# Kernel tuning notes

Measured on AMD Instinct MI355X. Metric: run time of the kernel, lower is better.

The kernel has to match this reference:

```python
import math
import jax, jax.numpy as jnp
import numpy as np

B, N, D = 16, 4096, 256
N_CAT, N_TPC, N_VPT, N_SP = 16, 8, 4, 16
N_TYPE = N_CAT * N_TPC          # 128
N_VAR = N_TYPE * N_VPT          # 512
THRESH = 0.1
MASK_VAL = jnp.finfo(jnp.float32).min / 2


def _linear(x, w, b):
    # torch nn.Linear: y = x @ W^T + b, W: (out, in)
    return x @ w.T + b


def _level(codes, proj_w, proj_b, K, X, mask, tau):
    """One codebook level: attention of codes over tokens.
    codes: (M, d). Returns H:(B,M,d), w_raw:(B,M)."""
    Q = _linear(codes, proj_w, proj_b)                       # (M, d)
    attn = jnp.einsum('md,bnd->bmn', Q, K) / math.sqrt(D)    # (B, M, N)
    attn = jnp.where(mask[:, None, :], attn, MASK_VAL)
    attn = jnp.clip(attn, -50.0, 50.0)
    G = jnp.nan_to_num(jax.nn.softmax(attn, axis=-1))        # (B, M, N)
    H = jnp.einsum('bmn,bnd->bmd', G, X)                     # (B, M, d)
    w_raw = jnp.linalg.norm(H, axis=-1) / tau                # (B, M)
    return H, w_raw


def _sparsify(w, thr):
    ws = jnp.where(w > thr, w, 0.0)
    return ws / (ws.sum(axis=-1, keepdims=True) + 1e-8)


def _forward(X, positions, category_codes, type_codes, variant_codes,
             spatial_codes, log_tau, cat_w, cat_b, type_w, type_b,
             var_w, var_b, sp_w, sp_b, k_w, k_b, g1_w, g1_b, g2_w, g2_b,
             out_w, out_b, ln_g, ln_b, level_weights, mask):
    tau = jnp.clip(jnp.exp(log_tau[0]) + 0.1, 0.1, 2.0)
    K = _linear(X, k_w, k_b)                                 # (B, N, d)

    # Level 0: category
    H_cat, w_cat_raw = _level(category_codes, cat_w, cat_b, K, X, mask, tau)
    w_cat = jax.nn.softmax(w_cat_raw, axis=-1)
    w_cat_sp = _sparsify(w_cat, THRESH)

    # Level 1: type, gated by category selection
    H_type, w_type_raw = _level(type_codes.reshape(-1, D), type_w, type_b,
                                K, X, mask, tau)
    w_t = (w_type_raw.reshape(-1, N_CAT, N_TPC) * w_cat_sp[:, :, None]
           ).reshape(-1, N_TYPE)
    w_type = jax.nn.softmax(w_t, axis=-1)
    w_type_sp = _sparsify(w_type, THRESH / 2)

    # Level 2: variant, gated by type selection
    H_var, w_var_raw = _level(variant_codes.reshape(-1, D), var_w, var_b,
                              K, X, mask, tau)
    w_type_exp = jnp.repeat(w_type_sp, N_VPT, axis=-1)       # (B, 512)
    w_var = jax.nn.softmax(w_var_raw * w_type_exp, axis=-1)
    w_var_sp = _sparsify(w_var, THRESH / 4)

    # Spatial level (independent)
    H_sp, w_sp_raw = _level(spatial_codes, sp_w, sp_b, K, X, mask, tau)
    w_sp = jax.nn.softmax(w_sp_raw, axis=-1)
    w_sp_sp = _sparsify(w_sp, THRESH)

    z_cat = jnp.einsum('bm,bmd->bd', w_cat_sp, H_cat)
    z_type = jnp.einsum('bm,bmd->bd', w_type_sp, H_type)
    z_var = jnp.einsum('bm,bmd->bd', w_var_sp, H_var)
    z_spatial = jnp.einsum('bm,bmd->bd', w_sp_sp, H_sp)

    # Position gating of category summary
    mask_f = mask.astype(X.dtype)[:, :, None]
    pos_pooled = (positions * mask_f).sum(1) / jnp.maximum(mask_f.sum(1), 1.0)
    gate_in = jnp.concatenate([z_cat, pos_pooled], axis=-1)  # (B, 2d)
    h = jax.nn.gelu(_linear(gate_in, g1_w, g1_b), approximate=False)
    pos_gate = jax.nn.sigmoid(_linear(h, g2_w, g2_b))
    z_cat = z_cat * pos_gate

    # Learned level combine + gated output projection
    lw = jax.nn.softmax(level_weights)
    z = (lw[0] * z_cat + lw[1] * z_type + lw[2] * z_var + lw[3] * z_spatial)
    z = _linear(z, out_w, out_b)
    mu = z.mean(-1, keepdims=True)
    var = z.var(-1, keepdims=True)
    z = (z - mu) / jnp.sqrt(var + 1e-5) * ln_g + ln_b
    return z


def setup_inputs() -> dict:
    key = jax.random.key(0)
    ks = jax.random.split(key, 32)
    s = 1.0 / math.sqrt(D)
    inp = {
        'X': jax.random.normal(ks[0], (B, N, D), jnp.float32),
        'positions': jax.random.normal(ks[1], (B, N, D), jnp.float32),
        'category_codes': jax.random.normal(ks[2], (N_CAT, D)) * 0.02,
        'type_codes': jax.random.normal(ks[3], (N_CAT, N_TPC, D)) * 0.02,
        'variant_codes': jax.random.normal(ks[4], (N_CAT, N_TPC, N_VPT, D)) * 0.02,
        'spatial_codes': jax.random.normal(ks[5], (N_SP, D)) * 0.02,
        'log_tau': jnp.zeros((1,), jnp.float32),
        'cat_w': jax.random.normal(ks[6], (D, D)) * s,
        'cat_b': jnp.zeros((D,)),
        'type_w': jax.random.normal(ks[7], (D, D)) * s,
        'type_b': jnp.zeros((D,)),
        'var_w': jax.random.normal(ks[8], (D, D)) * s,
        'var_b': jnp.zeros((D,)),
        'sp_w': jax.random.normal(ks[9], (D, D)) * s,
        'sp_b': jnp.zeros((D,)),
        'k_w': jax.random.normal(ks[10], (D, D)) * s,
        'k_b': jnp.zeros((D,)),
        'g1_w': jax.random.normal(ks[11], (D, 2 * D)) * s,
        'g1_b': jnp.zeros((D,)),
        'g2_w': jax.random.normal(ks[12], (D, D)) * s,
        'g2_b': jnp.zeros((D,)),
        'out_w': jax.random.normal(ks[13], (D, D)) * s,
        'out_b': jnp.zeros((D,)),
        'ln_g': jnp.ones((D,)),
        'ln_b': jnp.zeros((D,)),
        'level_weights': jnp.ones((4,)) / 4.0,
        'mask': jnp.ones((B, N), jnp.bool_),
    }
    return inp


def reference(X, positions, category_codes, type_codes, variant_codes,
              spatial_codes, log_tau, cat_w, cat_b, type_w, type_b,
              var_w, var_b, sp_w, sp_b, k_w, k_b, g1_w, g1_b, g2_w, g2_b,
              out_w, out_b, ln_g, ln_b, level_weights, mask):
    return _forward(X, positions, category_codes, type_codes, variant_codes,
                    spatial_codes, log_tau, cat_w, cat_b, type_w, type_b,
                    var_w, var_b, sp_w, sp_b, k_w, k_b, g1_w, g1_b,
                    g2_w, g2_b, out_w, out_b, ln_g, ln_b, level_weights, mask)
```

## Files before the change

### kernel.cpp

```cpp
#include <hip/hip_runtime.h>


#define DEV static __device__ __forceinline__

typedef short bf16x8 __attribute__((ext_vector_type(8)));
typedef float f32x4 __attribute__((ext_vector_type(4)));
typedef unsigned short u16x8 __attribute__((ext_vector_type(8)));

DEV float bf2f(unsigned short u) {
  return __uint_as_float(((unsigned int)u) << 16);
}
DEV unsigned short f2bf(float f) {
  unsigned int x = __float_as_uint(f);
  unsigned int r = (x + 0x7fffu + ((x >> 16) & 1u)) >> 16;
  return (unsigned short)r;
}

DEV void gl2lds16(const void* g, void* l) {
  __builtin_amdgcn_global_load_lds(
      (const __attribute__((address_space(1))) unsigned int*)g,
      (__attribute__((address_space(3))) unsigned int*)l, 16, 0, 0);
}

DEV bf16x8 pack8(const float4 a, const float4 b) {
  bf16x8 r;
  r[0] = (short)f2bf(a.x); r[1] = (short)f2bf(a.y);
  r[2] = (short)f2bf(a.z); r[3] = (short)f2bf(a.w);
  r[4] = (short)f2bf(b.x); r[5] = (short)f2bf(b.y);
  r[6] = (short)f2bf(b.z); r[7] = (short)f2bf(b.w);
  return r;
}

DEV size_t pk_off(int rt, int ks) { return ((size_t)rt * 8 + ks) * 512; }

__global__ __launch_bounds__(256) void kproj_mfma(
    const float* __restrict__ X, const float* __restrict__ W,
    const float* __restrict__ bias, unsigned short* __restrict__ Kp) {
  __shared__ __align__(16) unsigned short As[128 * 72];
  __shared__ __align__(16) unsigned short Bs[128 * 72];
  const int m0 = blockIdx.x * 128, c0 = blockIdx.y * 128;
  const int t = threadIdx.x, l = t & 63, w = t >> 6;
  const int wm = (w & 1) * 64, wn = (w >> 1) * 64;
  const f32x4 zero = {0.f, 0.f, 0.f, 0.f};
  f32x4 acc[4][4];
#pragma unroll
  for (int i = 0; i < 4; ++i)
#pragma unroll
    for (int j = 0; j < 4; ++j) acc[i][j] = zero;
  const int rr = t >> 3, cc = (t & 7) * 8;
  for (int kc = 0; kc < 256; kc += 64) {
    __syncthreads();
#pragma unroll
    for (int p = 0; p < 4; ++p) {
      const int r = p * 32 + rr;
      const float* xs = &X[(size_t)(m0 + r) * 256 + kc + cc];
      const float4 a0 = *(const float4*)&xs[0];
      const float4 a1 = *(const float4*)&xs[4];
      *(bf16x8*)&As[r * 72 + cc] = pack8(a0, a1);
      const float* wsrc = &W[(size_t)(c0 + r) * 256 + kc + cc];
      const float4 b0 = *(const float4*)&wsrc[0];
      const float4 b1 = *(const float4*)&wsrc[4];
      *(bf16x8*)&Bs[r * 72 + cc] = pack8(b0, b1);
    }
    __syncthreads();
#pragma unroll
    for (int ks = 0; ks < 2; ++ks) {
      const int koff = ks * 32 + ((l >> 4) & 3) * 8;
      bf16x8 a[4], b[4];
#pragma unroll
      for (int f = 0; f < 4; ++f)
        a[f] = *(const bf16x8*)&As[(wm + f * 16 + (l & 15)) * 72 + koff];
#pragma unroll
      for (int f = 0; f < 4; ++f)
        b[f] = *(const bf16x8*)&Bs[(wn + f * 16 + (l & 15)) * 72 + koff];
#pragma unroll
      for (int i = 0; i < 4; ++i)
#pragma unroll
        for (int j = 0; j < 4; ++j)
          acc[i][j] =
              __builtin_amdgcn_mfma_f32_16x16x32_bf16(a[i], b[j], acc[i][j],
                                                      0, 0, 0);
    }
  }
  const int q = (l >> 4) & 3;
#pragma unroll
  for (int j = 0; j < 4; ++j) {
    const int c = c0 + wn + j * 16 + (l & 15);
    const float bv = bias[c];
#pragma unroll
    for (int i = 0; i < 4; ++i) {
      const int mrow = m0 + wm + i * 16 + q * 4;
#pragma unroll
      for (int r = 0; r < 4; ++r) {
        const int m = mrow + r;
        Kp[pk_off(m >> 4, c >> 5) + ((m & 15) + 16 * ((c >> 3) & 3)) * 8 +
           (c & 7)] = f2bf(acc[i][j][r] + bv);
      }
    }
  }
}

__global__ __launch_bounds__(256) void xT_kern(const float* __restrict__ X,
                                               unsigned short* __restrict__ XTp) {
  __shared__ float Ls[64][65];
  const int tn = blockIdx.x, td = blockIdx.y, b = blockIdx.z;
  const int t = threadIdx.x;
  const int nl = t >> 2, dp = (t & 3) * 16;
  const float* src =
      X + ((size_t)b * 4096 + tn * 64 + nl) * 256 + td * 64 + dp;
#pragma unroll
  for (int v = 0; v < 4; ++v) {
    const float4 x = *(const float4*)&src[v * 4];
    Ls[nl][dp + v * 4 + 0] = x.x;
    Ls[nl][dp + v * 4 + 1] = x.y;
    Ls[nl][dp + v * 4 + 2] = x.z;
    Ls[nl][dp + v * 4 + 3] = x.w;
  }
  __syncthreads();
  const int dl = t >> 2, np = (t & 3) * 16;
  u16x8 h0, h1;
#pragma unroll
  for (int j = 0; j < 8; ++j) h0[j] = f2bf(Ls[np + j][dl]);
#pragma unroll
  for (int j = 0; j < 8; ++j) h1[j] = f2bf(Ls[np + 8 + j][dl]);
  const int d = td * 64 + dl;
  const int n0g = tn * 64 + np;
  const int n1g = n0g + 8;
  unsigned short* dst = XTp + (size_t)b * 1048576;
  const size_t o0 = (((size_t)(d >> 4) * 128) + (n0g >> 5)) * 512 +
                    ((d & 15) + 16 * ((n0g >> 3) & 3)) * 8;
  const size_t o1 = (((size_t)(d >> 4) * 128) + (n1g >> 5)) * 512 +
                    ((d & 15) + 16 * ((n1g >> 3) & 3)) * 8;
  *(u16x8*)&dst[o0] = h0;
  *(u16x8*)&dst[o1] = h1;
}

__global__ __launch_bounds__(256) void qproj_kern(
    const float* __restrict__ cat_codes, const float* __restrict__ type_codes,
    const float* __restrict__ var_codes, const float* __restrict__ sp_codes,
    const float* __restrict__ cat_w, const float* __restrict__ cat_b,
    const float* __restrict__ type_w, const float* __restrict__ type_b,
    const float* __restrict__ var_w, const float* __restrict__ var_b,
    const float* __restrict__ sp_w, const float* __restrict__ sp_b,
    unsigned short* __restrict__ Qp) {
  const int m = blockIdx.x;
  const int t = threadIdx.x;
  const size_t off = pk_off(m >> 4, t >> 5) +
                     ((m & 15) + 16 * ((t >> 3) & 3)) * 8 + (t & 7);
  if (m >= 672) {
    Qp[off] = 0;
    return;
  }
  const float* code;
  const float* W;
  const float* bias;
  if (m < 16)       { code = cat_codes  + m * 256;         W = cat_w;  bias = cat_b; }
  else if (m < 144) { code = type_codes + (m - 16) * 256;  W = type_w; bias = type_b; }
  else if (m < 656) { code = var_codes  + (m - 144) * 256; W = var_w;  bias = var_b; }
  else              { code = sp_codes   + (m - 656) * 256; W = sp_w;   bias = sp_b; }
  __shared__ float xs[256];
  xs[t] = code[t];
  __syncthreads();
  float a = bias[t];
  const float* wr = W + (size_t)t * 256;
  for (int k = 0; k < 256; k += 4) {
    const float4 w = *(const float4*)&wr[k];
    a = fmaf(w.x, xs[k], a);
    a = fmaf(w.y, xs[k + 1], a);
    a = fmaf(w.z, xs[k + 2], a);
    a = fmaf(w.w, xs[k + 3], a);
  }
  Qp[off] = f2bf(a);
}

__global__ __launch_bounds__(256, 2) void attn_fused(
    const unsigned short* __restrict__ Qp, const unsigned short* __restrict__ Kp,
    const unsigned short* __restrict__ XTp,
    const unsigned char* __restrict__ mask, float* __restrict__ H,
    float* __restrict__ lsum) {
  __shared__ __align__(16) unsigned short Ks[2][16384];
  __shared__ __align__(16) unsigned short Plds[64 * 72];
  __shared__ unsigned char msk[1024];
  const int combo = blockIdx.x;
  const int m0 = blockIdx.y * 64;
  const int b = combo >> 2;
  const int nbase = (combo & 3) * 1024;
  const int t = threadIdx.x, l = t & 63, w = t >> 6;
  const int l15 = l & 15, q = l >> 4;
  ((uchar4*)msk)[t] = ((const uchar4*)(mask + (size_t)b * 4096 + nbase))[t];
  const int mt_g = (m0 >> 4) + w;
  bf16x8 qf[8];
#pragma unroll
  for (int ks = 0; ks < 8; ++ks)
    qf[ks] = *(const bf16x8*)&Qp[pk_off(mt_g, ks) + l * 8];
  const f32x4 zero = {0.f, 0.f, 0.f, 0.f};
  f32x4 accO[4][4];
#pragma unroll
  for (int i = 0; i < 4; ++i)
#pragma unroll
    for (int j = 0; j < 4; ++j) accO[i][j] = zero;
  f32x4 rs = zero;
  const unsigned short* XTb = XTp + (size_t)b * 1048576;
  const unsigned short* Kchunk0 = Kp + ((size_t)b * 256 + (nbase >> 4)) * 4096;
#pragma unroll
  for (int i = 0; i < 8; ++i)
    gl2lds16(Kchunk0 + (w * 8 + i) * 512 + l * 8, &Ks[0][(w * 8 + i) * 512]);
  for (int c = 0; c < 16; ++c) {
    const int cur = c & 1;
    __syncthreads();
    const int nst0 = (nbase >> 5) + c * 2;
    bf16x8 xf[2][4];
#pragma unroll
    for (int ks2 = 0; ks2 < 2; ++ks2)
#pragma unroll
      for (int dj = 0; dj < 4; ++dj)
        xf[ks2][dj] = *(const bf16x8*)&XTb[((size_t)(4 * w + dj) * 128 +
                                            nst0 + ks2) * 512 + l * 8];
    f32x4 accS[4];
#pragma unroll
    for (int f = 0; f < 4; ++f) accS[f] = zero;
#pragma unroll
    for (int ks = 0; ks < 8; ++ks) {
      bf16x8 kf[4];
#pragma unroll
      for (int f = 0; f < 4; ++f)
        kf[f] = *(const bf16x8*)&Ks[cur][(f * 8 + ks) * 512 + l * 8];
#pragma unroll
      for (int f = 0; f < 4; ++f)
        accS[f] = __builtin_amdgcn_mfma_f32_16x16x32_bf16(qf[ks], kf[f],
                                                          accS[f], 0, 0, 0);
    }
#pragma unroll
    for (int f = 0; f < 4; ++f) {
      const bool mk = msk[c * 64 + f * 16 + l15] != 0;
#pragma unroll
      for (int r = 0; r < 4; ++r) {
        float s = accS[f][r] * 0.0625f;
        s = fminf(fmaxf(s, -50.f), 50.f);
        if (!mk) s = -50.f;
        const float e = __expf(s);
        Plds[(w * 16 + q * 4 + r) * 72 + f * 16 + l15] = f2bf(e);
        rs[r] += e;
      }
    }
    __syncthreads();
    if (c < 15) {
      const unsigned short* src = Kchunk0 + (size_t)(c + 1) * 16384;
      unsigned short* dst = &Ks[1 - cur][0];
#pragma unroll
      for (int i = 0; i < 8; ++i)
        gl2lds16(src + (w * 8 + i) * 512 + l * 8, dst + (w * 8 + i) * 512);
    }
#pragma unroll
    for (int ks2 = 0; ks2 < 2; ++ks2) {
      bf16x8 pf[4];
#pragma unroll
      for (int mt = 0; mt < 4; ++mt)
        pf[mt] = *(const bf16x8*)&Plds[(mt * 16 + l15) * 72 + ks2 * 32 + q * 8];
#pragma unroll
      for (int mt = 0; mt < 4; ++mt)
#pragma unroll
        for (int dj = 0; dj < 4; ++dj)
          accO[mt][dj] = __builtin_amdgcn_mfma_f32_16x16x32_bf16(
              pf[mt], xf[ks2][dj], accO[mt][dj], 0, 0, 0);
    }
  }
#pragma unroll
  for (int r = 0; r < 4; ++r) {
    float v = rs[r];
    v += __shfl_xor(v, 1, 64);
    v += __shfl_xor(v, 2, 64);
    v += __shfl_xor(v, 4, 64);
    v += __shfl_xor(v, 8, 64);
    const int m = m0 + w * 16 + q * 4 + r;
    if (l15 == 0 && m < 672) atomicAdd(&lsum[b * 672 + m], v);
  }
#pragma unroll
  for (int mt = 0; mt < 4; ++mt) {
    const int mbase = m0 + mt * 16 + q * 4;
#pragma unroll
    for (int dj = 0; dj < 4; ++dj) {
      const int d = w * 64 + dj * 16 + l15;
#pragma unroll
      for (int r = 0; r < 4; ++r) {
        const int m = mbase + r;
        if (m < 672)
          atomicAdd(&H[((size_t)b * 672 + m) * 256 + d], accO[mt][dj][r]);
      }
    }
  }
}

__global__ __launch_bounds__(256) void hfinal_ip(
    float* __restrict__ H, const float* __restrict__ lsum,
    const float* __restrict__ log_tau, float* __restrict__ wraw) {
  const int bm = blockIdx.x;
  const int t = threadIdx.x;
  __shared__ float red[256];
  const float inv = 1.0f / lsum[bm];
  const float v = H[(size_t)bm * 256 + t] * inv;
  H[(size_t)bm * 256 + t] = v;
  red[t] = v * v;
  __syncthreads();
  for (int s = 128; s > 0; s >>= 1) {
    if (t < s) red[t] += red[t + s];
    __syncthreads();
  }
  if (t == 0) {
    const float tau = fminf(fmaxf(expf(log_tau[0]) + 0.1f, 0.1f), 2.0f);
    wraw[bm] = sqrtf(red[0]) / tau;
  }
}

__global__ __launch_bounds__(256) void pospool_kern(
    const float* __restrict__ pos, const unsigned char* __restrict__ mask,
    float* __restrict__ pacc, float* __restrict__ cnt) {
  const int b = blockIdx.x, seg = blockIdx.y, t = threadIdx.x;
  const int dg = t & 63;
  const int nl = t >> 6;
  const int n0 = seg * 128;
  float4 acc = make_float4(0.f, 0.f, 0.f, 0.f);
  float c = 0.f;
  const float* pb = pos + (size_t)b * 4096 * 256;
  for (int j = 0; j < 32; ++j) {
    const int n = n0 + j * 4 + nl;
    const unsigned char mk = mask[(size_t)b * 4096 + n];
    if (mk) {
      const float4 v = *(const float4*)&pb[(size_t)n * 256 + dg * 4];
      acc.x += v.x; acc.y += v.y; acc.z += v.z; acc.w += v.w;
      if (dg == 0) c += 1.f;
    }
  }
  __shared__ float4 red4[256];
  __shared__ float redc[4];
  red4[t] = acc;
  if (dg == 0) redc[nl] = c;
  __syncthreads();
  if (t < 64) {
    float4 s = red4[t];
    const float4 s1 = red4[t + 64], s2 = red4[t + 128], s3 = red4[t + 192];
    s.x += s1.x + s2.x + s3.x;
    s.y += s1.y + s2.y + s3.y;
    s.z += s1.z + s2.z + s3.z;
    s.w += s1.w + s2.w + s3.w;
    float* pa = pacc + b * 256 + t * 4;
    atomicAdd(pa + 0, s.x);
    atomicAdd(pa + 1, s.y);
    atomicAdd(pa + 2, s.z);
    atomicAdd(pa + 3, s.w);
    if (t == 0) atomicAdd(&cnt[b], redc[0] + redc[1] + redc[2] + redc[3]);
  }
}

DEV float wave_max(float v) {
#pragma unroll
  for (int m = 1; m < 64; m <<= 1) v = fmaxf(v, __shfl_xor(v, m, 64));
  return v;
}
DEV float wave_sum(float v) {
#pragma unroll
  for (int m = 1; m < 64; m <<= 1) v += __shfl_xor(v, m, 64);
  return v;
}

__global__ __launch_bounds__(256) void combine_kern(
    const float* __restrict__ wraw, const float* __restrict__ H,
    float* __restrict__ zbuf) {
  const int b = blockIdx.x, t = threadIdx.x, l = t & 63;
  __shared__ float wr[672];
  __shared__ float wsp[672];
  for (int i = t; i < 672; i += 256) wr[i] = wraw[b * 672 + i];
  __syncthreads();
  {
    const float v = (l < 16) ? wr[l] : -1e30f;
    const float mx = wave_max(v);
    const float e = (l < 16) ? expf(wr[l] - mx) : 0.f;
    const float s = wave_sum(e);
    float w = e / s;
    w = (w > 0.1f) ? w : 0.f;
    const float s2 = wave_sum(w);
    if (l < 16) wsp[l] = w / (s2 + 1e-8f);
  }
  __syncthreads();
  {
    const float L0 = wr[16 + l] * wsp[l >> 3];
    const float L1 = wr[16 + 64 + l] * wsp[(64 + l) >> 3];
    const float mx = wave_max(fmaxf(L0, L1));
    const float e0 = expf(L0 - mx), e1 = expf(L1 - mx);
    const float s = wave_sum(e0 + e1);
    float w0 = e0 / s, w1 = e1 / s;
    w0 = (w0 > 0.05f) ? w0 : 0.f;
    w1 = (w1 > 0.05f) ? w1 : 0.f;
    const float s2 = wave_sum(w0 + w1);
    const float inv2 = 1.f / (s2 + 1e-8f);
    wsp[16 + l] = w0 * inv2;
    wsp[16 + 64 + l] = w1 * inv2;
  }
  __syncthreads();
  {
    float Lv[8];
    float lm = -1e30f;
#pragma unroll
    for (int j = 0; j < 8; ++j) {
      const int i = l * 8 + j;
      Lv[j] = wr[144 + i] * wsp[16 + (i >> 2)];
      lm = fmaxf(lm, Lv[j]);
    }
    const float mx = wave_max(lm);
    float ls = 0.f;
#pragma unroll
    for (int j = 0; j < 8; ++j) {
      Lv[j] = expf(Lv[j] - mx);
      ls += Lv[j];
    }
    const float s = wave_sum(ls);
    const float inv = 1.f / s;
    float ls2 = 0.f;
#pragma unroll
    for (int j = 0; j < 8; ++j) {
      float w = Lv[j] * inv;
      w = (w > 0.025f) ? w : 0.f;
      Lv[j] = w;
      ls2 += w;
    }
    const float s2 = wave_sum(ls2);
    const float inv2 = 1.f / (s2 + 1e-8f);
#pragma unroll
    for (int j = 0; j < 8; ++j) wsp[144 + l * 8 + j] = Lv[j] * inv2;
  }
  __syncthreads();
  {
    const float v = (l < 16) ? wr[656 + l] : -1e30f;
    const float mx = wave_max(v);
    const float e = (l < 16) ? expf(wr[656 + l] - mx) : 0.f;
    const float s = wave_sum(e);
    float w = e / s;
    w = (w > 0.1f) ? w : 0.f;
    const float s2 = wave_sum(w);
    if (l < 16) wsp[656 + l] = w / (s2 + 1e-8f);
  }
  __syncthreads();
  const float* Hb = H + (size_t)b * 672 * 256 + t;
  float z0 = 0.f, z1 = 0.f, z2 = 0.f, z3 = 0.f;
  for (int m = 0; m < 16; ++m) {
    const float wv = wsp[m];
    if (wv != 0.f) z0 = fmaf(wv, Hb[(size_t)m * 256], z0);
  }
  for (int m = 0; m < 128; ++m) {
    const float wv = wsp[16 + m];
    if (wv != 0.f) z1 = fmaf(wv, Hb[(size_t)(16 + m) * 256], z1);
  }
  for (int m = 0; m < 512; ++m) {
    const float wv = wsp[144 + m];
    if (wv != 0.f) z2 = fmaf(wv, Hb[(size_t)(144 + m) * 256], z2);
  }
  for (int m = 0; m < 16; ++m) {
    const float wv = wsp[656 + m];
    if (wv != 0.f) z3 = fmaf(wv, Hb[(size_t)(656 + m) * 256], z3);
  }
  zbuf[(b * 4 + 0) * 256 + t] = z0;
  zbuf[(b * 4 + 1) * 256 + t] = z1;
  zbuf[(b * 4 + 2) * 256 + t] = z2;
  zbuf[(b * 4 + 3) * 256 + t] = z3;
}

__global__ __launch_bounds__(256) void gate_kern(
    const float* __restrict__ zbuf, const float* __restrict__ pacc,
    const float* __restrict__ cnt, const float* __restrict__ g1_w,
    const float* __restrict__ g1_b, const float* __restrict__ g2_w,
    const float* __restrict__ g2_b, const float* __restrict__ out_w,
    const float* __restrict__ out_b, const float* __restrict__ ln_g,
    const float* __restrict__ ln_b, const float* __restrict__ lvlw,
    float* __restrict__ out) {
  const int b = blockIdx.x, t = threadIdx.x;
  __shared__ float gin[512];
  __shared__ float hb[256];
  __shared__ float zc[256];
  __shared__ float red[256];
  const float z0 = zbuf[(b * 4 + 0) * 256 + t];
  gin[t] = z0;
  const float c = fmaxf(cnt[b], 1.0f);
  gin[256 + t] = pacc[b * 256 + t] / c;
  __syncthreads();
  float a = g1_b[t];
  const float* w1 = g1_w + (size_t)t * 512;
  for (int k = 0; k < 512; k += 4) {
    const float4 w = *(const float4*)&w1[k];
    a = fmaf(w.x, gin[k], a);
    a = fmaf(w.y, gin[k + 1], a);
    a = fmaf(w.z, gin[k + 2], a);
    a = fmaf(w.w, gin[k + 3], a);
  }
  const float hg = 0.5f * a * (1.0f + erff(a * 0.7071067811865475f));
  hb[t] = hg;
  __syncthreads();
  float a2 = g2_b[t];
  const float* w2 = g2_w + (size_t)t * 256;
  for (int k = 0; k < 256; k += 4) {
    const float4 w = *(const float4*)&w2[k];
    a2 = fmaf(w.x, hb[k], a2);
    a2 = fmaf(w.y, hb[k + 1], a2);
    a2 = fmaf(w.z, hb[k + 2], a2);
    a2 = fmaf(w.w, hb[k + 3], a2);
  }
  const float pg = 1.0f / (1.0f + expf(-a2));
  const float l0 = lvlw[0], l1 = lvlw[1], l2 = lvlw[2], l3 = lvlw[3];
  const float mx = fmaxf(fmaxf(l0, l1), fmaxf(l2, l3));
  const float e0 = expf(l0 - mx), e1 = expf(l1 - mx);
  const float e2 = expf(l2 - mx), e3 = expf(l3 - mx);
  const float einv = 1.0f / (e0 + e1 + e2 + e3);
  const float zmix = (e0 * z0 * pg + e1 * zbuf[(b * 4 + 1) * 256 + t] +
                      e2 * zbuf[(b * 4 + 2) * 256 + t] +
                      e3 * zbuf[(b * 4 + 3) * 256 + t]) * einv;
  zc[t] = zmix;
  __syncthreads();
  float o = out_b[t];
  const float* wo = out_w + (size_t)t * 256;
  for (int k = 0; k < 256; k += 4) {
    const float4 w = *(const float4*)&wo[k];
    o = fmaf(w.x, zc[k], o);
    o = fmaf(w.y, zc[k + 1], o);
    o = fmaf(w.z, zc[k + 2], o);
    o = fmaf(w.w, zc[k + 3], o);
  }
  red[t] = o;
  __syncthreads();
  for (int s = 128; s > 0; s >>= 1) {
    if (t < s) red[t] += red[t + s];
    __syncthreads();
  }
  const float mu = red[0] / 256.f;
  __syncthreads();
  red[t] = o * o;
  __syncthreads();
  for (int s = 128; s > 0; s >>= 1) {
    if (t < s) red[t] += red[t + s];
    __syncthreads();
  }
  const float var = red[0] / 256.f - mu * mu;
  out[b * 256 + t] = (o - mu) * rsqrtf(var + 1e-5f) * ln_g[t] + ln_b[t];
}

extern "C" void kernel_launch(void* const* d_in, const int* in_sizes, int n_in,
                              void* d_out, int out_size, void* d_ws,
                              size_t ws_size, hipStream_t stream) {
  (void)in_sizes; (void)n_in; (void)out_size; (void)ws_size;
  const float* X          = (const float*)d_in[0];
  const float* positions  = (const float*)d_in[1];
  const float* cat_codes  = (const float*)d_in[2];
  const float* type_codes = (const float*)d_in[3];
  const float* var_codes  = (const float*)d_in[4];
  const float* sp_codes   = (const float*)d_in[5];
  const float* log_tau    = (const float*)d_in[6];
  const float* cat_w      = (const float*)d_in[7];
  const float* cat_b      = (const float*)d_in[8];
  const float* type_w     = (const float*)d_in[9];
  const float* type_b     = (const float*)d_in[10];
  const float* var_w      = (const float*)d_in[11];
  const float* var_b      = (const float*)d_in[12];
  const float* sp_w       = (const float*)d_in[13];
  const float* sp_b       = (const float*)d_in[14];
  const float* k_w        = (const float*)d_in[15];
  const float* k_b        = (const float*)d_in[16];
  const float* g1_w       = (const float*)d_in[17];
  const float* g1_b       = (const float*)d_in[18];
  const float* g2_w       = (const float*)d_in[19];
  const float* g2_b       = (const float*)d_in[20];
  const float* out_w      = (const float*)d_in[21];
  const float* out_b      = (const float*)d_in[22];
  const float* ln_g       = (const float*)d_in[23];
  const float* ln_b       = (const float*)d_in[24];
  const float* lvlw       = (const float*)d_in[25];
  const unsigned char* mask = (const unsigned char*)d_in[26];

  char* ws = (char*)d_ws;
  constexpr size_t O_KP  = 0;
  constexpr size_t O_XT  = 33554432;
  constexpr size_t O_QP  = 67108864;
  constexpr size_t O_H   = 67469312;
  constexpr size_t O_L   = 78479360;
  constexpr size_t O_WR  = 78522368;
  constexpr size_t O_PA  = 78565376;
  constexpr size_t O_CNT = 78581760;
  constexpr size_t O_Z   = 78581824;

  unsigned short* Kp  = (unsigned short*)(ws + O_KP);
  unsigned short* XTp = (unsigned short*)(ws + O_XT);
  unsigned short* Qp  = (unsigned short*)(ws + O_QP);
  float* H            = (float*)(ws + O_H);
  float* lsum         = (float*)(ws + O_L);
  float* wraw         = (float*)(ws + O_WR);
  float* pacc         = (float*)(ws + O_PA);
  float* cnt          = (float*)(ws + O_CNT);
  float* zbuf         = (float*)(ws + O_Z);
  float* out          = (float*)d_out;

  hipMemsetAsync(lsum, 0, 16 * 672 * 4, stream);
  hipMemsetAsync(H, 0, 11010048, stream);
  hipMemsetAsync(pacc, 0, 16 * 256 * 4, stream);
  hipMemsetAsync(cnt, 0, 64, stream);

  qproj_kern<<<dim3(704), 256, 0, stream>>>(
      cat_codes, type_codes, var_codes, sp_codes, cat_w, cat_b, type_w, type_b,
      var_w, var_b, sp_w, sp_b, Qp);
  kproj_mfma<<<dim3(512, 2), 256, 0, stream>>>(X, k_w, k_b, Kp);
  xT_kern<<<dim3(64, 4, 16), 256, 0, stream>>>(X, XTp);
  pospool_kern<<<dim3(16, 32), 256, 0, stream>>>(positions, mask, pacc, cnt);

  attn_fused<<<dim3(64, 11), 256, 0, stream>>>(Qp, Kp, XTp, mask, H, lsum);

  hfinal_ip<<<dim3(16 * 672), 256, 0, stream>>>(H, lsum, log_tau, wraw);
  combine_kern<<<dim3(16), 256, 0, stream>>>(wraw, H, zbuf);
  gate_kern<<<dim3(16), 256, 0, stream>>>(zbuf, pacc, cnt, g1_w, g1_b, g2_w,
                                          g2_b, out_w, out_b, ln_g, ln_b, lvlw,
                                          out);
}
```

Before: 451.2 us.

## Fold softmax normalisation into combine weights and split combine across blocks

Measured after the change: 424.8 us. 5.8% less time.

```diff
diff --git a/kernel.cpp b/kernel.cpp
--- a/kernel.cpp
+++ b/kernel.cpp
@@ -291,24 +291,19 @@
   }
 }
 
-__global__ __launch_bounds__(256) void hfinal_ip(
-    float* __restrict__ H, const float* __restrict__ lsum,
+__global__ __launch_bounds__(256) void hnorm_kern(
+    const float* __restrict__ H, const float* __restrict__ lsum,
     const float* __restrict__ log_tau, float* __restrict__ wraw) {
-  const int bm = blockIdx.x;
-  const int t = threadIdx.x;
-  __shared__ float red[256];
-  const float inv = 1.0f / lsum[bm];
-  const float v = H[(size_t)bm * 256 + t] * inv;
-  H[(size_t)bm * 256 + t] = v;
-  red[t] = v * v;
-  __syncthreads();
-  for (int s = 128; s > 0; s >>= 1) {
-    if (t < s) red[t] += red[t + s];
-    __syncthreads();
-  }
-  if (t == 0) {
+  const int b = blockIdx.x, j = blockIdx.y;
+  const int t = threadIdx.x, l = t & 63, w = t >> 6;
+  const int m = j * 4 + w;
+  const float4 v = *(const float4*)&H[((size_t)b * 672 + m) * 256 + l * 4];
+  float ss = v.x * v.x + v.y * v.y + v.z * v.z + v.w * v.w;
+#pragma unroll
+  for (int s = 1; s < 64; s <<= 1) ss += __shfl_xor(ss, s, 64);
+  if (l == 0) {
     const float tau = fminf(fmaxf(expf(log_tau[0]) + 0.1f, 0.1f), 2.0f);
-    wraw[bm] = sqrtf(red[0]) / tau;
+    wraw[b * 672 + m] = sqrtf(ss) / (lsum[b * 672 + m] * tau);
   }
 }
 
@@ -324,12 +319,13 @@
   const float* pb = pos + (size_t)b * 4096 * 256;
   for (int j = 0; j < 32; ++j) {
     const int n = n0 + j * 4 + nl;
-    const unsigned char mk = mask[(size_t)b * 4096 + n];
-    if (mk) {
-      const float4 v = *(const float4*)&pb[(size_t)n * 256 + dg * 4];
-      acc.x += v.x; acc.y += v.y; acc.z += v.z; acc.w += v.w;
-      if (dg == 0) c += 1.f;
-    }
+    const float mf = mask[(size_t)b * 4096 + n] ? 1.f : 0.f;
+    const float4 v = *(const float4*)&pb[(size_t)n * 256 + dg * 4];
+    acc.x = fmaf(mf, v.x, acc.x);
+    acc.y = fmaf(mf, v.y, acc.y);
+    acc.z = fmaf(mf, v.z, acc.z);
+    acc.w = fmaf(mf, v.w, acc.w);
+    c += mf;
   }
   __shared__ float4 red4[256];
   __shared__ float redc[4];
@@ -364,9 +360,9 @@
 }
 
 __global__ __launch_bounds__(256) void combine_kern(
-    const float* __restrict__ wraw, const float* __restrict__ H,
-    float* __restrict__ zbuf) {
-  const int b = blockIdx.x, t = threadIdx.x, l = t & 63;
+    const float* __restrict__ wraw, const float* __restrict__ lsum,
+    const float* __restrict__ H, float* __restrict__ zbuf) {
+  const int b = blockIdx.x, j = blockIdx.y, t = threadIdx.x, l = t & 63;
   __shared__ float wr[672];
   __shared__ float wsp[672];
   for (int i = t; i < 672; i += 256) wr[i] = wraw[b * 672 + i];
@@ -401,32 +397,32 @@
     float Lv[8];
     float lm = -1e30f;
 #pragma unroll
-    for (int j = 0; j < 8; ++j) {
-      const int i = l * 8 + j;
-      Lv[j] = wr[144 + i] * wsp[16 + (i >> 2)];
-      lm = fmaxf(lm, Lv[j]);
+    for (int jj = 0; jj < 8; ++jj) {
+      const int i = l * 8 + jj;
+      Lv[jj] = wr[144 + i] * wsp[16 + (i >> 2)];
+      lm = fmaxf(lm, Lv[jj]);
     }
     const float mx = wave_max(lm);
     float ls = 0.f;
 #pragma unroll
-    for (int j = 0; j < 8; ++j) {
-      Lv[j] = expf(Lv[j] - mx);
-      ls += Lv[j];
+    for (int jj = 0; jj < 8; ++jj) {
+      Lv[jj] = expf(Lv[jj] - mx);
+      ls += Lv[jj];
     }
     const float s = wave_sum(ls);
     const float inv = 1.f / s;
     float ls2 = 0.f;
 #pragma unroll
-    for (int j = 0; j < 8; ++j) {
-      float w = Lv[j] * inv;
+    for (int jj = 0; jj < 8; ++jj) {
+      float w = Lv[jj] * inv;
       w = (w > 0.025f) ? w : 0.f;
-      Lv[j] = w;
+      Lv[jj] = w;
       ls2 += w;
     }
     const float s2 = wave_sum(ls2);
     const float inv2 = 1.f / (s2 + 1e-8f);
 #pragma unroll
-    for (int j = 0; j < 8; ++j) wsp[144 + l * 8 + j] = Lv[j] * inv2;
+    for (int jj = 0; jj < 8; ++jj) wsp[144 + l * 8 + jj] = Lv[jj] * inv2;
   }
   __syncthreads();
   {
@@ -440,28 +436,22 @@
     if (l < 16) wsp[656 + l] = w / (s2 + 1e-8f);
   }
   __syncthreads();
+  for (int i = t; i < 672; i += 256) wsp[i] = wsp[i] / lsum[b * 672 + i];
+  __syncthreads();
   const float* Hb = H + (size_t)b * 672 * 256 + t;
-  float z0 = 0.f, z1 = 0.f, z2 = 0.f, z3 = 0.f;
-  for (int m = 0; m < 16; ++m) {
-    const float wv = wsp[m];
-    if (wv != 0.f) z0 = fmaf(wv, Hb[(size_t)m * 256], z0);
-  }
-  for (int m = 0; m < 128; ++m) {
-    const float wv = wsp[16 + m];
-    if (wv != 0.f) z1 = fmaf(wv, Hb[(size_t)(16 + m) * 256], z1);
-  }
-  for (int m = 0; m < 512; ++m) {
-    const float wv = wsp[144 + m];
-    if (wv != 0.f) z2 = fmaf(wv, Hb[(size_t)(144 + m) * 256], z2);
-  }
-  for (int m = 0; m < 16; ++m) {
-    const float wv = wsp[656 + m];
-    if (wv != 0.f) z3 = fmaf(wv, Hb[(size_t)(656 + m) * 256], z3);
-  }
-  zbuf[(b * 4 + 0) * 256 + t] = z0;
-  zbuf[(b * 4 + 1) * 256 + t] = z1;
-  zbuf[(b * 4 + 2) * 256 + t] = z2;
-  zbuf[(b * 4 + 3) * 256 + t] = z3;
+  const int s0 = j * 84, s1 = s0 + 84;
+  const int Llo[4] = {0, 16, 144, 656};
+  const int Lhi[4] = {16, 144, 656, 672};
+#pragma unroll
+  for (int lv = 0; lv < 4; ++lv) {
+    const int lo = max(s0, Llo[lv]);
+    const int hi = min(s1, Lhi[lv]);
+    if (lo >= hi) continue;
+    float z = 0.f;
+    for (int m = lo; m < hi; ++m)
+      z = fmaf(wsp[m], Hb[(size_t)m * 256], z);
+    atomicAdd(&zbuf[(b * 4 + lv) * 256 + t], z);
+  }
 }
 
 __global__ __launch_bounds__(256) void gate_kern(
@@ -599,6 +589,7 @@
   hipMemsetAsync(H, 0, 11010048, stream);
   hipMemsetAsync(pacc, 0, 16 * 256 * 4, stream);
   hipMemsetAsync(cnt, 0, 64, stream);
+  hipMemsetAsync(zbuf, 0, 16 * 4 * 256 * 4, stream);
 
   qproj_kern<<<dim3(704), 256, 0, stream>>>(
       cat_codes, type_codes, var_codes, sp_codes, cat_w, cat_b, type_w, type_b,
@@ -609,8 +600,8 @@
 
   attn_fused<<<dim3(64, 11), 256, 0, stream>>>(Qp, Kp, XTp, mask, H, lsum);
 
-  hfinal_ip<<<dim3(16 * 672), 256, 0, stream>>>(H, lsum, log_tau, wraw);
-  combine_kern<<<dim3(16), 256, 0, stream>>>(wraw, H, zbuf);
+  hnorm_kern<<<dim3(16, 168), 256, 0, stream>>>(H, lsum, log_tau, wraw);
+  combine_kern<<<dim3(16, 8), 256, 0, stream>>>(wraw, lsum, H, zbuf);
   gate_kern<<<dim3(16), 256, 0, stream>>>(zbuf, pacc, cnt, g1_w, g1_b, g2_w,
                                           g2_b, out_w, out_b, ln_g, ln_b, lvlw,
                                           out);
```
